# Optimization experiments

Measured on AMD Instinct MI355X. Metric: run time of the kernel, lower is better.

## Reference

```python
import jax, jax.numpy as jnp
import numpy as np


def bilinear_align_corners(p, H, W):
    # p: [B, C, h, w] -> [B, C, H, W], matches F.interpolate(mode='bilinear', align_corners=True)
    b, c, h, w = p.shape
    ys = jnp.linspace(0.0, h - 1.0, H)
    xs = jnp.linspace(0.0, w - 1.0, W)
    y0 = jnp.floor(ys).astype(jnp.int32)
    x0 = jnp.floor(xs).astype(jnp.int32)
    y1 = jnp.minimum(y0 + 1, h - 1)
    x1 = jnp.minimum(x0 + 1, w - 1)
    wy = (ys - y0.astype(p.dtype))[:, None]          # [H,1]
    wx = (xs - x0.astype(p.dtype))                   # [W]
    rows = p[:, :, y0, :] * (1 - wy) + p[:, :, y1, :] * wy   # [B,C,H,w]
    out = rows[:, :, :, x0] * (1 - wx) + rows[:, :, :, x1] * wx  # [B,C,H,W]
    return out


def conv1x1(x, W, b):
    return jnp.einsum('bchw,oc->bohw', x, W) + b[None, :, None, None]


def scan_axis(feat, A_bar, B_bar, axis):
    # selective recurrence h_i = A_i * stop_grad(h_{i-1}) + B_i * x_i along `axis`
    f = jnp.moveaxis(feat, axis, 0)
    A = jnp.moveaxis(A_bar, axis, 0)
    B = jnp.moveaxis(B_bar, axis, 0)

    def step(prev, inp):
        a_i, b_i, x_i = inp
        h = a_i * jax.lax.stop_gradient(prev) + b_i * x_i
        return h, h

    _, hs = jax.lax.scan(step, jnp.zeros_like(f[0]), (A, B, f))
    return jnp.moveaxis(hs, 0, axis)


def setup_inputs() -> dict:
    key = jax.random.key(0)
    ks = jax.random.split(key, 12)
    Bsz, Cin, H, W = 4, 64, 256, 256
    hid = 128
    s_in = 1.0 / np.sqrt(Cin)
    s_hid = 1.0 / np.sqrt(hid)
    return {
        'x': jax.random.normal(ks[0], (Bsz, Cin, H, W), jnp.float32),
        'prior': jax.random.normal(ks[1], (Bsz, 1, 64, 64), jnp.float32),
        'W_in': jax.random.uniform(ks[2], (hid, Cin), jnp.float32, -s_in, s_in),
        'b_in': jax.random.uniform(ks[3], (hid,), jnp.float32, -s_in, s_in),
        'W_out': jax.random.uniform(ks[4], (Cin, hid), jnp.float32, -s_hid, s_hid),
        'b_out': jax.random.uniform(ks[5], (Cin,), jnp.float32, -s_hid, s_hid),
        'W_delta': jax.random.uniform(ks[6], (hid, hid), jnp.float32, -s_hid, s_hid),
        'b_delta': jax.random.uniform(ks[7], (hid,), jnp.float32, -s_hid, s_hid),
        'W_B': jax.random.uniform(ks[8], (hid, hid), jnp.float32, -s_hid, s_hid),
        'b_B': jax.random.uniform(ks[9], (hid,), jnp.float32, -s_hid, s_hid),
        'A_param': jax.random.normal(ks[10], (hid,), jnp.float32),
        'lambda_delta': jnp.float32(0.1),
        'alpha': jnp.float32(0.1),
        'gamma': jnp.float32(0.1),
    }


def reference(x, prior, W_in, b_in, W_out, b_out, W_delta, b_delta, W_B, b_B,
              A_param, lambda_delta, alpha, gamma):
    Bsz, C, H, W = x.shape
    prior_up = jnp.clip(bilinear_align_corners(prior, H, W), -1.0, 1.0)
    x_proj = conv1x1(x, W_in, b_in)
    delta = jax.nn.softplus(conv1x1(x_proj, W_delta, b_delta) + lambda_delta * prior_up)
    B_k = conv1x1(x_proj, W_B, b_B) * (1.0 + alpha * prior_up)
    A = -jnp.exp(A_param)[None, :, None, None]
    A_bar = jnp.exp(delta * A)
    B_bar = delta * B_k
    # dim=0 in torch code scans along W (axis 3); dim=1 scans along H (axis 2)
    scanned = scan_axis(x_proj, A_bar, B_bar, 3) + scan_axis(x_proj, A_bar, B_bar, 2)
    out = conv1x1(scanned, W_out, b_out)
    return (x + gamma * out, prior_up)
```

## Files before the change

kernel.cpp:

```cpp
#include <hip/hip_runtime.h>
#include <hip/hip_bf16.h>

#define OUT1 16777216
#define BIG  33554432

typedef _Float16 half8 __attribute__((ext_vector_type(8)));
typedef float    floatx4 __attribute__((ext_vector_type(4)));

struct __align__(8) h4s { _Float16 x, y, z, w; };
__device__ inline void store4h(_Float16* p, float4 v){
    h4s t; t.x = (_Float16)v.x; t.y = (_Float16)v.y; t.z = (_Float16)v.z; t.w = (_Float16)v.w;
    *(h4s*)p = t;
}

__global__ __launch_bounds__(256) void k_prior(const float* __restrict__ prior, float* __restrict__ pu){
    int i = blockIdx.x*256 + threadIdx.x;
    int b = i >> 16;
    int rem = i & 65535;
    int yy = rem >> 8, xx = rem & 255;
    const float scale = 63.0f/255.0f;
    float sy = yy*scale, sx = xx*scale;
    int y0 = min((int)floorf(sy), 63), x0 = min((int)floorf(sx), 63);
    int y1 = min(y0+1, 63), x1 = min(x0+1, 63);
    float wy = sy - (float)y0, wx = sx - (float)x0;
    const float* pb = prior + (b<<12);
    float v00 = pb[(y0<<6)+x0], v01 = pb[(y0<<6)+x1];
    float v10 = pb[(y1<<6)+x0], v11 = pb[(y1<<6)+x1];
    float r0 = v00*(1.f-wy) + v10*wy;
    float r1 = v01*(1.f-wy) + v11*wy;
    float v  = r0*(1.f-wx) + r1*wx;
    pu[i] = fminf(fmaxf(v, -1.f), 1.f);
}

__global__ __launch_bounds__(256) void k_comb(const float* __restrict__ W_in, const float* __restrict__ b_in,
        const float* __restrict__ W_delta, const float* __restrict__ b_delta,
        const float* __restrict__ W_B, const float* __restrict__ b_B,
        const float* __restrict__ A_param, const float* __restrict__ W_out,
        _Float16* __restrict__ Wch, float* __restrict__ bcv, float* __restrict__ negA,
        _Float16* __restrict__ Wof){
    int i = blockIdx.x*256 + threadIdx.x;
    if (i < 24576){
        int r = i >> 6, c = i & 63;
        float v;
        if (r < 128) v = W_in[i];
        else if (r < 256){
            int rr = r-128; float s = 0.f;
            for (int k=0;k<128;k++) s = fmaf(W_delta[(rr<<7)+k], W_in[(k<<6)+c], s);
            v = s;
        } else {
            int rr = r-256; float s = 0.f;
            for (int k=0;k<128;k++) s = fmaf(W_B[(rr<<7)+k], W_in[(k<<6)+c], s);
            v = s;
        }
        Wch[i] = (_Float16)v;
    } else if (i < 24960){
        int r = i - 24576; float v;
        if (r < 128) v = b_in[r];
        else if (r < 256){
            int rr=r-128; float s = b_delta[rr];
            for (int k=0;k<128;k++) s = fmaf(W_delta[(rr<<7)+k], b_in[k], s);
            v = s;
        } else {
            int rr=r-256; float s = b_B[rr];
            for (int k=0;k<128;k++) s = fmaf(W_B[(rr<<7)+k], b_in[k], s);
            v = s;
        }
        bcv[r] = v;
    } else if (i < 25088){
        negA[i-24960] = -expf(A_param[i-24960]);
    } else if (i < 33280){
        Wof[i-25088] = (_Float16)W_out[i-25088];
    }
}

__global__ __launch_bounds__(256, 2) void k_proj_mfma(const float* __restrict__ x, const float* __restrict__ pu,
        const _Float16* __restrict__ Wch, const float* __restrict__ bcv, const float* __restrict__ negA,
        const float* __restrict__ lam_p, const float* __restrict__ alp_p,
        _Float16* __restrict__ Ab, _Float16* __restrict__ Uu){
    __shared__ _Float16 Ws[384][72];

    const int t    = threadIdx.x;
    const int lane = t & 63;
    const int wave = t >> 6;
    const int col  = lane & 15;
    const int quad = lane >> 4;

    const int blk = blockIdx.x;
    const int b   = blk >> 10;
    const int p0  = (blk & 1023) << 6;
    const int pxw = p0 + (wave << 4);

    {
        const float4* wsrc = (const float4*)Wch;
        #pragma unroll
        for (int i = 0; i < 12; i++){
            int c = t + i*256;
            int row = c >> 3, part = c & 7;
            float4 v = wsrc[c];
            *(float4*)&Ws[row][part<<3] = v;
        }
    }

    const float* xb = x + ((size_t)b<<22) + pxw + col;
    half8 aX[2];
    #pragma unroll
    for (int kh = 0; kh < 2; kh++){
        half8 h;
        #pragma unroll
        for (int j = 0; j < 8; j++){
            int k = kh*32 + quad*8 + j;
            h[j] = (_Float16)xb[(size_t)k<<16];
        }
        aX[kh] = h;
    }
    __syncthreads();

    floatx4 acc[24];
    #pragma unroll
    for (int nt = 0; nt < 24; nt++){
        half8 b0 = *(const half8*)&Ws[nt*16 + col][quad*8];
        half8 b1 = *(const half8*)&Ws[nt*16 + col][32 + quad*8];
        floatx4 a = (floatx4){0.f,0.f,0.f,0.f};
        a = __builtin_amdgcn_mfma_f32_16x16x32_f16(aX[0], b0, a, 0, 0, 0);
        a = __builtin_amdgcn_mfma_f32_16x16x32_f16(aX[1], b1, a, 0, 0, 0);
        acc[nt] = a;
    }

    const float lamv = lam_p[0], alpv = alp_p[0];
    float4 puv4 = *(const float4*)(pu + (b<<16) + pxw + (quad<<2));
    float lpu[4], apu[4];
    #pragma unroll
    for (int r = 0; r < 4; r++){
        float pv = ((const float*)&puv4)[r];
        lpu[r] = lamv * pv;
        apu[r] = fmaf(alpv, pv, 1.f);
    }
    #pragma unroll
    for (int ct = 0; ct < 8; ct++){
        int c = (ct<<4) + col;
        float bI = bcv[c], bD = bcv[128+c], bB = bcv[256+c], nA = negA[c];
        floatx4 aI = acc[ct], aD = acc[8+ct], aB = acc[16+ct];
        h4s oa, ou;
        #pragma unroll
        for (int r = 0; r < 4; r++){
            float sI = aI[r] + bI;
            float sD = aD[r] + bD;
            float sB = aB[r] + bB;
            float dpre  = sD + lpu[r];
            float delta = fmaxf(dpre, 0.f) + __logf(1.f + __expf(-fabsf(dpre)));
            float ab    = __expf(nA * delta);
            float uu    = delta * sB * apu[r] * sI;
            (&oa.x)[r] = (_Float16)ab;
            (&ou.x)[r] = (_Float16)uu;
        }
        size_t o = ((size_t)((b<<7) + c)<<16) + pxw + (quad<<2);
        *(h4s*)(Ab+o) = oa;
        *(h4s*)(Uu+o) = ou;
    }
}

__global__ __launch_bounds__(256) void k_scan_w(const _Float16* __restrict__ Ab, const _Float16* __restrict__ Uu,
                                                _Float16* __restrict__ Sw){
    int r    = (blockIdx.x<<2) + (threadIdx.x>>6);
    int lane = threadIdx.x & 63;
    size_t base = ((size_t)r<<8) + (lane<<2);
    h4s a4 = *(const h4s*)(Ab+base);
    h4s u4 = *(const h4s*)(Uu+base);
    float ax=(float)a4.x, ay=(float)a4.y, az=(float)a4.z, aw=(float)a4.w;
    float ux=(float)u4.x, uy=(float)u4.y, uz=(float)u4.z, uw=(float)u4.w;
    float A = ax, U = ux;
    U = fmaf(ay, U, uy); A *= ay;
    U = fmaf(az, U, uz); A *= az;
    U = fmaf(aw, U, uw); A *= aw;
    #pragma unroll
    for (int off=1; off<64; off<<=1){
        float Apv = __shfl_up(A, off, 64);
        float Upv = __shfl_up(U, off, 64);
        if (lane >= off){ U = fmaf(A, Upv, U); A *= Apv; }
    }
    float h = __shfl_up(U, 1, 64);
    if (lane == 0) h = 0.f;
    float4 o;
    h = fmaf(ax, h, ux); o.x = h;
    h = fmaf(ay, h, uy); o.y = h;
    h = fmaf(az, h, uz); o.z = h;
    h = fmaf(aw, h, uw); o.w = h;
    store4h(Sw+base, o);
}

__global__ __launch_bounds__(256) void k_scan_h(const _Float16* __restrict__ AbH, const _Float16* __restrict__ UuH,
                                                const _Float16* __restrict__ Sw, _Float16* __restrict__ Sh){
    int t   = blockIdx.x*256 + threadIdx.x;
    int col = t >> 8;
    int w   = t & 255;
    size_t base = ((size_t)col<<16) + w;
    float h = 0.f;
    #pragma unroll 4
    for (int hh=0; hh<256; hh++){
        size_t idx = base + ((size_t)hh<<8);
        float a = (float)AbH[idx];
        float u = (float)UuH[idx];
        float s = (float)Sw[idx];
        h = fmaf(a, h, u);
        Sh[idx] = (_Float16)(h + s);
    }
}

__global__ __launch_bounds__(256, 2) void k_out_mfma(const float* __restrict__ x, const _Float16* __restrict__ Sh,
        const _Float16* __restrict__ Wof, const float* __restrict__ bout, const float* __restrict__ gam_p,
        float* __restrict__ out){
    const int t    = threadIdx.x;
    const int lane = t & 63;
    const int wave = t >> 6;
    const int col  = lane & 15;
    const int quad = lane >> 4;
    const int b    = blockIdx.x >> 8;
    const int p0   = (blockIdx.x & 255) << 8;
    const int wn0  = wave << 6;

    const _Float16* shb = Sh + ((size_t)b<<23) + p0;

    floatx4 acc[4][4];
    #pragma unroll
    for (int mt = 0; mt < 4; mt++)
        #pragma unroll
        for (int nt = 0; nt < 4; nt++)
            acc[mt][nt] = (floatx4){0.f,0.f,0.f,0.f};

    #pragma unroll
    for (int kc = 0; kc < 4; kc++){
        half8 bf[4];
        #pragma unroll
        for (int nt = 0; nt < 4; nt++){
            int px = wn0 + nt*16 + col;
            #pragma unroll
            for (int j = 0; j < 8; j++)
                bf[nt][j] = shb[((size_t)(kc*32 + quad*8 + j)<<16) + px];
        }
        half8 af[4];
        #pragma unroll
        for (int mt = 0; mt < 4; mt++)
            af[mt] = *(const half8*)(Wof + (mt*16 + col)*128 + kc*32 + quad*8);
        #pragma unroll
        for (int mt = 0; mt < 4; mt++)
            #pragma unroll
            for (int nt = 0; nt < 4; nt++)
                acc[mt][nt] = __builtin_amdgcn_mfma_f32_16x16x32_f16(af[mt], bf[nt], acc[mt][nt], 0, 0, 0);
    }

    const float gv = gam_p[0];
    #pragma unroll
    for (int mt = 0; mt < 4; mt++){
        #pragma unroll
        for (int nt = 0; nt < 4; nt++){
            int px = wn0 + nt*16 + col;
            #pragma unroll
            for (int r = 0; r < 4; r++){
                int o = mt*16 + quad*4 + r;
                size_t idx = (((size_t)(b*64 + o))<<16) + p0 + px;
                out[idx] = fmaf(gv, acc[mt][nt][r] + bout[o], x[idx]);
            }
        }
    }
}

extern "C" void kernel_launch(void* const* d_in, const int* in_sizes, int n_in,
                              void* d_out, int out_size, void* d_ws, size_t ws_size,
                              hipStream_t stream){
    const float* x       = (const float*)d_in[0];
    const float* prior   = (const float*)d_in[1];
    const float* W_in    = (const float*)d_in[2];
    const float* b_in    = (const float*)d_in[3];
    const float* W_out   = (const float*)d_in[4];
    const float* b_out   = (const float*)d_in[5];
    const float* W_delta = (const float*)d_in[6];
    const float* b_delta = (const float*)d_in[7];
    const float* W_B     = (const float*)d_in[8];
    const float* b_B     = (const float*)d_in[9];
    const float* A_param = (const float*)d_in[10];
    const float* lam     = (const float*)d_in[11];
    const float* alp     = (const float*)d_in[12];
    const float* gam     = (const float*)d_in[13];

    float* out = (float*)d_out;
    float* pu  = out + OUT1;

    float* ws        = (float*)d_ws;
    _Float16* Wch    = (_Float16*)ws;
    float* bcv       = ws + 12288;
    float* negA      = ws + 12672;
    _Float16* Wof    = (_Float16*)(ws + 12800);
    _Float16* AbH    = (_Float16*)(ws + 32768);
    _Float16* UuH    = AbH + BIG;
    _Float16* Sh     = UuH + BIG;
    _Float16* Sw     = (_Float16*)out;

    hipLaunchKernelGGL(k_prior,  dim3(1024),  dim3(256), 0, stream, prior, pu);
    hipLaunchKernelGGL(k_comb,   dim3(130),   dim3(256), 0, stream, W_in, b_in, W_delta, b_delta,
                       W_B, b_B, A_param, W_out, Wch, bcv, negA, Wof);
    hipLaunchKernelGGL(k_proj_mfma, dim3(4096), dim3(256), 0, stream,
                       x, pu, Wch, bcv, negA, lam, alp, AbH, UuH);
    hipLaunchKernelGGL(k_scan_w, dim3(32768), dim3(256), 0, stream, AbH, UuH, Sw);
    hipLaunchKernelGGL(k_scan_h, dim3(512),   dim3(256), 0, stream, AbH, UuH, Sw, Sh);
    hipLaunchKernelGGL(k_out_mfma, dim3(1024), dim3(256), 0, stream, x, Sh, Wof, b_out, gam, out);
}
```

Measured before the change: 327.5 us.

## Drop LDS weight staging in projection, swap MFMA operands in output GEMM

The projection kernel no longer copies the 384x64 weight tile into shared memory. Each channel tile now loads its weight fragments straight from global memory inside a non-unrolled loop, which removes the 24-accumulator array, lowers register use and lets launch bounds rise to 6 blocks. The output kernel swaps the A/B MFMA operands so each lane's accumulator holds 4 consecutive pixels, which enables float4 loads of x and float4 stores of out, and its occupancy hint rises to 4. The cost is repeated weight reads from global/L2 per block and a serialized MFMA chain per channel tile.

Result: slower. 376.1 us (+14.8%).

```diff
diff --git a/kernel.cpp b/kernel.cpp
--- a/kernel.cpp
+++ b/kernel.cpp
@@ -73,12 +73,10 @@
     }
 }
 
-__global__ __launch_bounds__(256, 2) void k_proj_mfma(const float* __restrict__ x, const float* __restrict__ pu,
+__global__ __launch_bounds__(256, 6) void k_proj_mfma(const float* __restrict__ x, const float* __restrict__ pu,
         const _Float16* __restrict__ Wch, const float* __restrict__ bcv, const float* __restrict__ negA,
         const float* __restrict__ lam_p, const float* __restrict__ alp_p,
         _Float16* __restrict__ Ab, _Float16* __restrict__ Uu){
-    __shared__ _Float16 Ws[384][72];
-
     const int t    = threadIdx.x;
     const int lane = t & 63;
     const int wave = t >> 6;
@@ -90,40 +88,12 @@
     const int p0  = (blk & 1023) << 6;
     const int pxw = p0 + (wave << 4);
 
-    {
-        const float4* wsrc = (const float4*)Wch;
-        #pragma unroll
-        for (int i = 0; i < 12; i++){
-            int c = t + i*256;
-            int row = c >> 3, part = c & 7;
-            float4 v = wsrc[c];
-            *(float4*)&Ws[row][part<<3] = v;
-        }
-    }
-
     const float* xb = x + ((size_t)b<<22) + pxw + col;
-    half8 aX[2];
-    #pragma unroll
-    for (int kh = 0; kh < 2; kh++){
-        half8 h;
-        #pragma unroll
-        for (int j = 0; j < 8; j++){
-            int k = kh*32 + quad*8 + j;
-            h[j] = (_Float16)xb[(size_t)k<<16];
-        }
-        aX[kh] = h;
-    }
-    __syncthreads();
-
-    floatx4 acc[24];
-    #pragma unroll
-    for (int nt = 0; nt < 24; nt++){
-        half8 b0 = *(const half8*)&Ws[nt*16 + col][quad*8];
-        half8 b1 = *(const half8*)&Ws[nt*16 + col][32 + quad*8];
-        floatx4 a = (floatx4){0.f,0.f,0.f,0.f};
-        a = __builtin_amdgcn_mfma_f32_16x16x32_f16(aX[0], b0, a, 0, 0, 0);
-        a = __builtin_amdgcn_mfma_f32_16x16x32_f16(aX[1], b1, a, 0, 0, 0);
-        acc[nt] = a;
+    half8 aX0, aX1;
+    #pragma unroll
+    for (int j = 0; j < 8; j++){
+        aX0[j] = (_Float16)xb[(size_t)(quad*8 + j) << 16];
+        aX1[j] = (_Float16)xb[(size_t)(quad*8 + j + 32) << 16];
     }
 
     const float lamv = lam_p[0], alpv = alp_p[0];
@@ -135,17 +105,37 @@
         lpu[r] = lamv * pv;
         apu[r] = fmaf(alpv, pv, 1.f);
     }
-    #pragma unroll
+
+    const _Float16* wrow = Wch + ((size_t)col << 6) + (quad << 3);
+
+    #pragma unroll 1
     for (int ct = 0; ct < 8; ct++){
+        const _Float16* w0 = wrow + (ct << 10);
+        half8 wI0 = *(const half8*)(w0);
+        half8 wI1 = *(const half8*)(w0 + 32);
+        half8 wD0 = *(const half8*)(w0 + 8192);
+        half8 wD1 = *(const half8*)(w0 + 8192 + 32);
+        half8 wB0 = *(const half8*)(w0 + 16384);
+        half8 wB1 = *(const half8*)(w0 + 16384 + 32);
+
+        floatx4 aI = (floatx4){0.f,0.f,0.f,0.f};
+        floatx4 aD = (floatx4){0.f,0.f,0.f,0.f};
+        floatx4 aB = (floatx4){0.f,0.f,0.f,0.f};
+        aI = __builtin_amdgcn_mfma_f32_16x16x32_f16(aX0, wI0, aI, 0, 0, 0);
+        aD = __builtin_amdgcn_mfma_f32_16x16x32_f16(aX0, wD0, aD, 0, 0, 0);
+        aB = __builtin_amdgcn_mfma_f32_16x16x32_f16(aX0, wB0, aB, 0, 0, 0);
+        aI = __builtin_amdgcn_mfma_f32_16x16x32_f16(aX1, wI1, aI, 0, 0, 0);
+        aD = __builtin_amdgcn_mfma_f32_16x16x32_f16(aX1, wD1, aD, 0, 0, 0);
+        aB = __builtin_amdgcn_mfma_f32_16x16x32_f16(aX1, wB1, aB, 0, 0, 0);
+
         int c = (ct<<4) + col;
-        float bI = bcv[c], bD = bcv[128+c], bB = bcv[256+c], nA = negA[c];
-        floatx4 aI = acc[ct], aD = acc[8+ct], aB = acc[16+ct];
+        float bI = bcv[c], bD = bcv[128+c], bBv = bcv[256+c], nA = negA[c];
         h4s oa, ou;
         #pragma unroll
         for (int r = 0; r < 4; r++){
             float sI = aI[r] + bI;
             float sD = aD[r] + bD;
-            float sB = aB[r] + bB;
+            float sB = aB[r] + bBv;
             float dpre  = sD + lpu[r];
             float delta = fmaxf(dpre, 0.f) + __logf(1.f + __expf(-fabsf(dpre)));
             float ab    = __expf(nA * delta);
@@ -206,7 +196,7 @@
     }
 }
 
-__global__ __launch_bounds__(256, 2) void k_out_mfma(const float* __restrict__ x, const _Float16* __restrict__ Sh,
+__global__ __launch_bounds__(256, 4) void k_out_mfma(const float* __restrict__ x, const _Float16* __restrict__ Sh,
         const _Float16* __restrict__ Wof, const float* __restrict__ bout, const float* __restrict__ gam_p,
         float* __restrict__ out){
     const int t    = threadIdx.x;
@@ -218,7 +208,7 @@
     const int p0   = (blockIdx.x & 255) << 8;
     const int wn0  = wave << 6;
 
-    const _Float16* shb = Sh + ((size_t)b<<23) + p0;
+    const _Float16* shb = Sh + ((size_t)b<<23) + p0 + wn0;
 
     floatx4 acc[4][4];
     #pragma unroll
@@ -229,18 +219,16 @@
 
     #pragma unroll
     for (int kc = 0; kc < 4; kc++){
-        half8 bf[4];
-        #pragma unroll
-        for (int nt = 0; nt < 4; nt++){
-            int px = wn0 + nt*16 + col;
+        half8 af[4];
+        #pragma unroll
+        for (int mt = 0; mt < 4; mt++)
             #pragma unroll
             for (int j = 0; j < 8; j++)
-                bf[nt][j] = shb[((size_t)(kc*32 + quad*8 + j)<<16) + px];
-        }
-        half8 af[4];
-        #pragma unroll
-        for (int mt = 0; mt < 4; mt++)
-            af[mt] = *(const half8*)(Wof + (mt*16 + col)*128 + kc*32 + quad*8);
+                af[mt][j] = shb[((size_t)(kc*32 + quad*8 + j)<<16) + mt*16 + col];
+        half8 bf[4];
+        #pragma unroll
+        for (int nt = 0; nt < 4; nt++)
+            bf[nt] = *(const half8*)(Wof + (nt*16 + col)*128 + kc*32 + quad*8);
         #pragma unroll
         for (int mt = 0; mt < 4; mt++)
             #pragma unroll
@@ -250,16 +238,19 @@
 
     const float gv = gam_p[0];
     #pragma unroll
-    for (int mt = 0; mt < 4; mt++){
-        #pragma unroll
-        for (int nt = 0; nt < 4; nt++){
-            int px = wn0 + nt*16 + col;
-            #pragma unroll
-            for (int r = 0; r < 4; r++){
-                int o = mt*16 + quad*4 + r;
-                size_t idx = (((size_t)(b*64 + o))<<16) + p0 + px;
-                out[idx] = fmaf(gv, acc[mt][nt][r] + bout[o], x[idx]);
-            }
+    for (int nt = 0; nt < 4; nt++){
+        int o = nt*16 + col;
+        float bo = bout[o];
+        #pragma unroll
+        for (int mt = 0; mt < 4; mt++){
+            size_t idx = (((size_t)(b*64 + o))<<16) + p0 + wn0 + mt*16 + (quad<<2);
+            float4 xv = *(const float4*)(x + idx);
+            float4 ov;
+            ov.x = fmaf(gv, acc[mt][nt][0] + bo, xv.x);
+            ov.y = fmaf(gv, acc[mt][nt][1] + bo, xv.y);
+            ov.z = fmaf(gv, acc[mt][nt][2] + bo, xv.z);
+            ov.w = fmaf(gv, acc[mt][nt][3] + bo, xv.w);
+            *(float4*)(out + idx) = ov;
         }
     }
 }
```
